# Performance work log

Measured on AMD Instinct MI355X. Metric: run time of the kernel, lower is better.

## Reference

```python
import jax, jax.numpy as jnp
import numpy as np

B, IN_DIM, H, E, V, MAX_LEN = 512, 1024, 512, 512, 2048, 32


def setup_inputs() -> dict:
    key = jax.random.key(0)
    ks = jax.random.split(key, 12)
    s = lambda k, shape, scale: (jax.random.normal(k, shape, dtype=jnp.float32) * scale)
    return {
        'x': jax.random.normal(ks[0], (B, IN_DIM), dtype=jnp.float32),
        'agent_w': s(ks[1], (IN_DIM, H), 1.0 / np.sqrt(IN_DIM)),
        'agent_b': jnp.zeros((H,), jnp.float32),
        'sos_embedding': s(ks[2], (E,), 0.01),  # reset_parameters: normal(0, 0.01)
        'embedding': s(ks[3], (V, E), 1.0),
        'w_ih': s(ks[4], (E, 4 * H), 1.0 / np.sqrt(H)),
        'w_hh': s(ks[5], (H, 4 * H), 1.0 / np.sqrt(H)),
        'b_ih': jnp.zeros((4 * H,), jnp.float32),
        'b_hh': jnp.zeros((4 * H,), jnp.float32),
        'out_w': s(ks[6], (H, V), 1.0 / np.sqrt(H)),
        'out_b': jnp.zeros((V,), jnp.float32),
    }


def _unroll(x, agent_w, agent_b, sos_embedding, embedding, w_ih, w_hh, b_ih, b_hh, out_w, out_b):
    h0 = x @ agent_w + agent_b              # agent provides initial hidden [B, H]
    c0 = jnp.zeros_like(h0)
    e0 = jnp.broadcast_to(sos_embedding, (x.shape[0], sos_embedding.shape[0]))
    key0 = jax.random.key(1)

    def step(carry, _):
        h, c, e, key = carry
        key, sk = jax.random.split(key)
        gates = e @ w_ih + h @ w_hh + (b_ih + b_hh)          # [B, 4H], torch gate order i,f,g,o
        i_g, f_g, g_g, o_g = jnp.split(gates, 4, axis=-1)
        c = jax.nn.sigmoid(f_g) * c + jax.nn.sigmoid(i_g) * jnp.tanh(g_g)
        h = jax.nn.sigmoid(o_g) * jnp.tanh(c)
        step_logits = jax.nn.log_softmax(h @ out_w + out_b, axis=-1)  # [B, V]
        probs = jnp.exp(step_logits)
        entropy = -jnp.sum(probs * step_logits, axis=-1)              # Categorical entropy
        sym = jax.random.categorical(sk, step_logits, axis=-1)        # sample [B]
        log_prob = jnp.take_along_axis(step_logits, sym[:, None], axis=1)[:, 0]
        e = embedding[sym]
        return (h, c, e, key), (sym, log_prob, entropy, probs)

    _, (seq, logp, ent, probs) = jax.lax.scan(step, (h0, c0, e0, key0), None, length=MAX_LEN)
    # scan emits leading time dim -> [B, L, ...]
    seq = jnp.transpose(seq, (1, 0))
    logp = jnp.transpose(logp, (1, 0))
    ent = jnp.transpose(ent, (1, 0))
    probs = jnp.transpose(probs, (1, 0, 2))
    # append EOS step (zeros; probs row of ones, as in the source)
    zcol = jnp.zeros((seq.shape[0], 1), jnp.float32)
    seq = jnp.concatenate([seq, zcol.astype(seq.dtype)], axis=1)
    logp = jnp.concatenate([logp, zcol], axis=1)
    ent = jnp.concatenate([ent, zcol], axis=1)
    probs = jnp.concatenate([probs, jnp.ones((probs.shape[0], 1, probs.shape[2]), probs.dtype)], axis=1)
    return seq, probs, logp, ent


def reference(x, agent_w, agent_b, sos_embedding, embedding, w_ih, w_hh, b_ih, b_hh, out_w, out_b):
    return _unroll(x, agent_w, agent_b, sos_embedding, embedding, w_ih, w_hh, b_ih, b_hh, out_w, out_b)
```

## Files before the change

kernel.cpp:

```cpp
#include <hip/hip_runtime.h>
#include <math.h>
#include <stdint.h>
#include <stddef.h>

#define B_ 512
#define H_ 512
#define E_ 512
#define V_ 2048
#define IN_ 1024
#define LSTEPS 32
#define LP1 33

#define TF_PARTITIONABLE 1

typedef unsigned short u16;
typedef __attribute__((ext_vector_type(8))) short bhalf8;
typedef __attribute__((ext_vector_type(4))) float f32x4;

__device__ __forceinline__ void tf2x32(uint32_t k0, uint32_t k1,
                                       uint32_t x0, uint32_t x1,
                                       uint32_t& o0, uint32_t& o1) {
  uint32_t ks2 = k0 ^ k1 ^ 0x1BD11BDAu;
  x0 += k0; x1 += k1;
#define TFR(R) { x0 += x1; x1 = (x1 << (R)) | (x1 >> (32 - (R))); x1 ^= x0; }
  TFR(13) TFR(15) TFR(26) TFR(6)
  x0 += k1; x1 += ks2 + 1u;
  TFR(17) TFR(29) TFR(16) TFR(24)
  x0 += ks2; x1 += k0 + 2u;
  TFR(13) TFR(15) TFR(26) TFR(6)
  x0 += k0; x1 += k1 + 3u;
  TFR(17) TFR(29) TFR(16) TFR(24)
  x0 += k1; x1 += ks2 + 4u;
  TFR(13) TFR(15) TFR(26) TFR(6)
  x0 += ks2; x1 += k0 + 5u;
#undef TFR
  o0 = x0; o1 = x1;
}

__global__ void init_keys_kernel(uint32_t* __restrict__ sk) {
  uint32_t k0 = 0u, k1 = 1u;
  for (int t = 0; t < LSTEPS; t++) {
    uint32_t a0, a1, b0, b1;
#if TF_PARTITIONABLE
    tf2x32(k0, k1, 0u, 0u, a0, a1);
    tf2x32(k0, k1, 0u, 1u, b0, b1);
    sk[2 * t] = b0; sk[2 * t + 1] = b1;
    k0 = a0; k1 = a1;
#else
    tf2x32(k0, k1, 0u, 2u, a0, a1);
    tf2x32(k0, k1, 1u, 3u, b0, b1);
    sk[2 * t] = a1; sk[2 * t + 1] = b1;
    k0 = a0; k1 = b0;
#endif
  }
}

__device__ __forceinline__ void split3(float v, u16& h, u16& m, u16& l) {
  uint32_t u = __float_as_uint(v);
  uint32_t r = (u + 0x7FFFu + ((u >> 16) & 1u)) >> 16;
  h = (u16)r;
  float res = v - __uint_as_float(r << 16);
  uint32_t u2 = __float_as_uint(res);
  uint32_t r2 = (u2 + 0x7FFFu + ((u2 >> 16) & 1u)) >> 16;
  m = (u16)r2;
  float res2 = res - __uint_as_float(r2 << 16);
  uint32_t u3 = __float_as_uint(res2);
  uint32_t r3 = (u3 + 0x7FFFu + ((u3 >> 16) & 1u)) >> 16;
  l = (u16)r3;
}

__global__ __launch_bounds__(256) void init_state_planes_kernel(
    const float* __restrict__ sos, float* __restrict__ c,
    u16* __restrict__ eh, u16* __restrict__ em, u16* __restrict__ el) {
  int idx = blockIdx.x * 256 + threadIdx.x;
  if (idx < B_ * H_) {
    c[idx] = 0.0f;
    u16 a, b2, d;
    split3(sos[idx & (E_ - 1)], a, b2, d);
    eh[idx] = a; em[idx] = b2; el[idx] = d;
  }
}

__global__ __launch_bounds__(256) void eos_fill_kernel(
    float* __restrict__ o_seq, float* __restrict__ o_probs,
    float* __restrict__ o_logp, float* __restrict__ o_ent) {
  int b = blockIdx.x, tid = threadIdx.x;
  float* pr = o_probs + ((size_t)b * LP1 + LSTEPS) * V_;
  for (int v = tid; v < V_; v += 256) pr[v] = 1.0f;
  if (tid == 0) {
    o_seq[b * LP1 + LSTEPS] = 0.0f;
    o_logp[b * LP1 + LSTEPS] = 0.0f;
    o_ent[b * LP1 + LSTEPS] = 0.0f;
  }
}

__global__ __launch_bounds__(256) void split_kernel(
    const float* __restrict__ src,
    u16* __restrict__ dh, u16* __restrict__ dm, u16* __restrict__ dl, int n) {
  int i = blockIdx.x * 256 + threadIdx.x;
  if (i < n) {
    u16 a, b2, d;
    split3(src[i], a, b2, d);
    dh[i] = a; dm[i] = b2; dl[i] = d;
  }
}

__global__ __launch_bounds__(256) void transpose_split_kernel(
    const float* __restrict__ src, int srcN,
    u16* __restrict__ dh, u16* __restrict__ dm, u16* __restrict__ dl,
    int dstK, int kOff) {
  __shared__ float t[32][33];
  int tx = threadIdx.x & 31, ty = threadIdx.x >> 5;
  int kt = blockIdx.x * 32, nt = blockIdx.y * 32;
#pragma unroll
  for (int j = 0; j < 4; j++)
    t[ty + j * 8][tx] = src[(size_t)(kt + ty + j * 8) * srcN + nt + tx];
  __syncthreads();
#pragma unroll
  for (int j = 0; j < 4; j++) {
    int n = nt + ty + j * 8;
    int k = kt + tx;
    u16 a, b2, d;
    split3(t[tx][ty + j * 8], a, b2, d);
    size_t o = (size_t)n * dstK + kOff + k;
    dh[o] = a; dm[o] = b2; dl[o] = d;
  }
}

typedef __attribute__((address_space(1))) const void GASV;
typedef __attribute__((address_space(3))) void LASV;
__device__ __forceinline__ void gld16(const void* g, void* l) {
  __builtin_amdgcn_global_load_lds((GASV*)g, (LASV*)l, 16, 0, 0);
}

__global__ __launch_bounds__(256, 3) void gemm64_kernel(
    const u16* __restrict__ A0h, const u16* __restrict__ A0m, const u16* __restrict__ A0l,
    const u16* __restrict__ A1h, const u16* __restrict__ A1m, const u16* __restrict__ A1l,
    int strideA, int kHalf,
    const u16* __restrict__ Bh, const u16* __restrict__ Bm, const u16* __restrict__ Bl,
    int strideB, int N, int K, int gridN,
    float* __restrict__ C) {
  __shared__ __align__(16) char lds[2][24576];
  int tid = threadIdx.x;
  int w = tid >> 6, l = tid & 63;
  int bid = blockIdx.x;
  int xcd = bid & 7, mIdx = (bid >> 3) & 7, cIdx = bid >> 6;
  int nIdx = xcd * (gridN >> 3) + cIdx;
  int m0 = mIdx * 64, n0 = nIdx * 64;

  int srow = l >> 2;
  int slog = (l & 3) ^ ((l >> 3) & 3);
  size_t aRow = (size_t)(m0 + w * 16 + srow) * strideA + slog * 8;
  size_t bRow = (size_t)(n0 + w * 16 + srow) * strideB + slog * 8;

  int lrow = l & 15, lk8 = l >> 4;
  int xorv = (lrow >> 1) & 3;
  int wr = (w >> 1) * 32, wc = (w & 1) * 32;
  int fOffA = (wr + lrow) * 64 + ((lk8 ^ xorv) << 4);
  int fOffB = (wc + lrow) * 64 + ((lk8 ^ xorv) << 4);

  f32x4 acc[2][2] = {};
  int nch = K >> 5;

#define STAGE64(CH, TB) {                                               \
    int kc = (CH) << 5;                                                 \
    bool hi2 = kc >= kHalf;                                             \
    const u16* Ah2 = hi2 ? A1h : A0h;                                   \
    const u16* Am2 = hi2 ? A1m : A0m;                                   \
    const u16* Al2 = hi2 ? A1l : A0l;                                   \
    size_t ao = aRow + (hi2 ? kc - kHalf : kc);                         \
    size_t bo = bRow + kc;                                              \
    char* Lb = (char*)&lds[TB][0] + w * 1024;                           \
    gld16(Ah2 + ao, Lb + 0 * 4096);                                     \
    gld16(Am2 + ao, Lb + 1 * 4096);                                     \
    gld16(Al2 + ao, Lb + 2 * 4096);                                     \
    gld16(Bh + bo, Lb + 3 * 4096);                                      \
    gld16(Bm + bo, Lb + 4 * 4096);                                      \
    gld16(Bl + bo, Lb + 5 * 4096);                                      \
  }

  STAGE64(0, 0)
  for (int ch = 0; ch < nch; ch++) {
    __syncthreads();
    if (ch + 1 < nch) STAGE64(ch + 1, (ch + 1) & 1)
    const char* base = (const char*)&lds[ch & 1][0];
    bhalf8 af[3][2], bfr[3][2];
#pragma unroll
    for (int p = 0; p < 3; p++) {
#pragma unroll
      for (int m = 0; m < 2; m++)
        af[p][m] = *(const bhalf8*)(base + p * 4096 + fOffA + m * 1024);
#pragma unroll
      for (int n = 0; n < 2; n++)
        bfr[p][n] = *(const bhalf8*)(base + (3 + p) * 4096 + fOffB + n * 1024);
    }
    const int PA[6] = {2, 0, 1, 1, 0, 0};
    const int PB[6] = {0, 2, 1, 0, 1, 0};
#pragma unroll
    for (int pp = 0; pp < 6; pp++) {
#pragma unroll
      for (int m = 0; m < 2; m++) {
#pragma unroll
        for (int n = 0; n < 2; n++) {
          acc[m][n] = __builtin_amdgcn_mfma_f32_16x16x32_bf16(
              af[PA[pp]][m], bfr[PB[pp]][n], acc[m][n], 0, 0, 0);
        }
      }
    }
  }
#undef STAGE64

#pragma unroll
  for (int m = 0; m < 2; m++) {
#pragma unroll
    for (int n = 0; n < 2; n++) {
#pragma unroll
      for (int j = 0; j < 4; j++) {
        int row = m0 + wr + m * 16 + lk8 * 4 + j;
        int col = n0 + wc + n * 16 + lrow;
        C[(size_t)row * N + col] = acc[m][n][j];
      }
    }
  }
}

__device__ __forceinline__ float sigm(float x) { return 1.0f / (1.0f + expf(-x)); }

__global__ __launch_bounds__(256) void cell_reduce_planes_kernel(
    const float* __restrict__ G,
    const float* __restrict__ b_ih, const float* __restrict__ b_hh,
    float* __restrict__ c,
    u16* __restrict__ hh_, u16* __restrict__ hm_, u16* __restrict__ hl_) {
  int idx = blockIdx.x * 256 + threadIdx.x;
  int b = idx >> 7;
  int h4 = (idx & 127) * 4;
  float4 g4[4];
#pragma unroll
  for (int g = 0; g < 4; g++) {
    size_t off = (size_t)b * 2048 + g * 512 + h4;
    float4 s = *(const float4*)&G[off];
    float4 bi = *(const float4*)&b_ih[g * 512 + h4];
    float4 bh = *(const float4*)&b_hh[g * 512 + h4];
    s.x += bi.x + bh.x; s.y += bi.y + bh.y; s.z += bi.z + bh.z; s.w += bi.w + bh.w;
    g4[g] = s;
  }
  size_t ci = (size_t)b * 512 + h4;
  float4 cold = *(const float4*)&c[ci];
  float4 cn;
  float hv[4];
  {
    const float* ig = (const float*)&g4[0];
    const float* fg = (const float*)&g4[1];
    const float* gg = (const float*)&g4[2];
    const float* og = (const float*)&g4[3];
    float* cc = (float*)&cn;
    const float* co = (const float*)&cold;
#pragma unroll
    for (int k = 0; k < 4; k++) {
      float cv = sigm(fg[k]) * co[k] + sigm(ig[k]) * tanhf(gg[k]);
      cc[k] = cv;
      hv[k] = sigm(og[k]) * tanhf(cv);
    }
  }
  *(float4*)&c[ci] = cn;
  ushort4 vh, vm, vl;
  u16 a, b2, d;
  split3(hv[0], a, b2, d); vh.x = a; vm.x = b2; vl.x = d;
  split3(hv[1], a, b2, d); vh.y = a; vm.y = b2; vl.y = d;
  split3(hv[2], a, b2, d); vh.z = a; vm.z = b2; vl.z = d;
  split3(hv[3], a, b2, d); vh.w = a; vm.w = b2; vl.w = d;
  *(ushort4*)&hh_[ci] = vh;
  *(ushort4*)&hm_[ci] = vm;
  *(ushort4*)&hl_[ci] = vl;
}

__global__ __launch_bounds__(256) void reduce_bias_planes_kernel(
    const float* __restrict__ P, int pstride, int nsplit,
    const float* __restrict__ bias,
    u16* __restrict__ oh, u16* __restrict__ om, u16* __restrict__ ol) {
  int idx = blockIdx.x * 256 + threadIdx.x;
  if (idx >= B_ * H_ / 4) return;
  size_t off = (size_t)idx * 4;
  float4 s = *(const float4*)&P[off];
  for (int sgl = 1; sgl < nsplit; sgl++) {
    float4 p = *(const float4*)&P[(size_t)sgl * pstride + off];
    s.x += p.x; s.y += p.y; s.z += p.z; s.w += p.w;
  }
  int col = (int)(off & (H_ - 1));
  float4 bv = *(const float4*)&bias[col];
  s.x += bv.x; s.y += bv.y; s.z += bv.z; s.w += bv.w;
  ushort4 vh, vm, vl;
  u16 a, b2, d;
  split3(s.x, a, b2, d); vh.x = a; vm.x = b2; vl.x = d;
  split3(s.y, a, b2, d); vh.y = a; vm.y = b2; vl.y = d;
  split3(s.z, a, b2, d); vh.z = a; vm.z = b2; vl.z = d;
  split3(s.w, a, b2, d); vh.w = a; vm.w = b2; vl.w = d;
  *(ushort4*)&oh[off] = vh;
  *(ushort4*)&om[off] = vm;
  *(ushort4*)&ol[off] = vl;
}

__global__ __launch_bounds__(256) void sample_step_kernel(
    const float* __restrict__ Z, const float* __restrict__ out_b,
    const uint32_t* __restrict__ skv,
    const u16* __restrict__ ebH, const u16* __restrict__ ebM, const u16* __restrict__ ebL,
    u16* __restrict__ eh, u16* __restrict__ em_, u16* __restrict__ el_,
    float* __restrict__ o_seq, float* __restrict__ o_probs,
    float* __restrict__ o_logp, float* __restrict__ o_ent, int t) {
  __shared__ float zs[V_];
  __shared__ float rmax[4], rsum[4], rps[4], rav[4];
  __shared__ int rai[4];
  int tid = threadIdx.x, b = blockIdx.x;
  int wid = tid >> 6;
  const float* pr0 = Z + (size_t)b * V_ + tid * 8;
  float4 za = *(const float4*)pr0;
  float4 zb = *(const float4*)(pr0 + 4);
  {
    float4 oa = *(const float4*)(out_b + tid * 8);
    float4 ob = *(const float4*)(out_b + tid * 8 + 4);
    za.x += oa.x; za.y += oa.y; za.z += oa.z; za.w += oa.w;
    zb.x += ob.x; zb.y += ob.y; zb.z += ob.z; zb.w += ob.w;
  }
  float zv[8] = {za.x, za.y, za.z, za.w, zb.x, zb.y, zb.z, zb.w};
  *(float4*)&zs[tid * 8] = za;
  *(float4*)&zs[tid * 8 + 4] = zb;

  float m = zv[0];
#pragma unroll
  for (int i = 1; i < 8; i++) m = fmaxf(m, zv[i]);
  for (int off = 32; off; off >>= 1) m = fmaxf(m, __shfl_xor(m, off));
  if ((tid & 63) == 0) rmax[wid] = m;
  __syncthreads();
  m = fmaxf(fmaxf(rmax[0], rmax[1]), fmaxf(rmax[2], rmax[3]));

  float sh[8];
  float ssum = 0.f;
#pragma unroll
  for (int i = 0; i < 8; i++) { sh[i] = zv[i] - m; ssum += expf(sh[i]); }
  for (int off = 32; off; off >>= 1) ssum += __shfl_xor(ssum, off);
  if ((tid & 63) == 0) rsum[wid] = ssum;
  __syncthreads();
  float S = (rsum[0] + rsum[1]) + (rsum[2] + rsum[3]);
  float ls = logf(S);

  uint32_t sk0 = skv[2 * t], sk1 = skv[2 * t + 1];
  float psum = 0.f;
  float best = -INFINITY;
  int bi = 0;
  float pv[8];
#pragma unroll
  for (int i = 0; i < 8; i++) {
    float s = sh[i] - ls;
    float p = expf(s);
    pv[i] = p;
    psum += p * s;
    int v = tid * 8 + i;
    uint32_t o0, o1, bits;
#if TF_PARTITIONABLE
    uint32_t j = (uint32_t)(b * V_ + v);
    tf2x32(sk0, sk1, 0u, j, o0, o1);
    bits = o0 ^ o1;
#else
    uint32_t j = (uint32_t)(b * V_ + v);
    const uint32_t n2 = (uint32_t)(B_ * V_ / 2);
    if (j < n2) { tf2x32(sk0, sk1, j, j + n2, o0, o1); bits = o0; }
    else       { tf2x32(sk0, sk1, j - n2, j, o0, o1); bits = o1; }
#endif
    float f = __uint_as_float((bits >> 9) | 0x3f800000u) - 1.0f;
    float u = fmaxf(f, 1.17549435e-38f);
    float g = -logf(-logf(u));
    float a = s + g;
    if (a > best) { best = a; bi = v; }
  }
  float* prw = o_probs + ((size_t)b * LP1 + t) * V_ + tid * 8;
  *(float4*)prw = make_float4(pv[0], pv[1], pv[2], pv[3]);
  *(float4*)(prw + 4) = make_float4(pv[4], pv[5], pv[6], pv[7]);

  for (int off = 32; off; off >>= 1) psum += __shfl_xor(psum, off);
  for (int off = 32; off; off >>= 1) {
    float ov = __shfl_xor(best, off);
    int oi = __shfl_xor(bi, off);
    if (ov > best || (ov == best && oi < bi)) { best = ov; bi = oi; }
  }
  if ((tid & 63) == 0) { rps[wid] = psum; rav[wid] = best; rai[wid] = bi; }
  __syncthreads();
  float ent = -((rps[0] + rps[1]) + (rps[2] + rps[3]));
  float bv2 = rav[0]; int sym = rai[0];
#pragma unroll
  for (int w2 = 1; w2 < 4; w2++) {
    if (rav[w2] > bv2 || (rav[w2] == bv2 && rai[w2] < sym)) { bv2 = rav[w2]; sym = rai[w2]; }
  }
  const u16* gh = ebH + (size_t)sym * E_;
  const u16* gm = ebM + (size_t)sym * E_;
  const u16* gl = ebL + (size_t)sym * E_;
  for (int k2 = tid; k2 < E_; k2 += 256) {
    eh[(size_t)b * E_ + k2]  = gh[k2];
    em_[(size_t)b * E_ + k2] = gm[k2];
    el_[(size_t)b * E_ + k2] = gl[k2];
  }
  if (tid == 0) {
    float s_sym = (zs[sym] - m) - ls;
    o_seq[b * LP1 + t] = (float)sym;
    o_logp[b * LP1 + t] = s_sym;
    o_ent[b * LP1 + t] = ent;
  }
}

extern "C" void kernel_launch(void* const* d_in, const int* in_sizes, int n_in,
                              void* d_out, int out_size, void* d_ws, size_t ws_size,
                              hipStream_t stream) {
  (void)in_sizes; (void)n_in; (void)out_size; (void)ws_size;
  const float* x     = (const float*)d_in[0];
  const float* agw   = (const float*)d_in[1];
  const float* agb   = (const float*)d_in[2];
  const float* sos   = (const float*)d_in[3];
  const float* emb   = (const float*)d_in[4];
  const float* w_ih  = (const float*)d_in[5];
  const float* w_hh  = (const float*)d_in[6];
  const float* b_ih  = (const float*)d_in[7];
  const float* b_hh  = (const float*)d_in[8];
  const float* out_w = (const float*)d_in[9];
  const float* out_b = (const float*)d_in[10];

  char* w = (char*)d_ws;
  size_t o = 0;
  uint32_t* sk = (uint32_t*)(w + o); o += 1024;
  float* c = (float*)(w + o);        o += (size_t)B_ * H_ * 4;
#define PLANE3(name, elems) \
  u16* name##H = (u16*)(w + o); o += (size_t)(elems) * 2; \
  u16* name##M = (u16*)(w + o); o += (size_t)(elems) * 2; \
  u16* name##L = (u16*)(w + o); o += (size_t)(elems) * 2;
  PLANE3(e,  B_ * E_)
  PLANE3(hA, B_ * H_)
  PLANE3(hB, B_ * H_)
  PLANE3(xp, B_ * IN_)
  PLANE3(aw, H_ * IN_)
  PLANE3(gw, 2048 * IN_)
  PLANE3(ow, V_ * H_)
  PLANE3(eb, V_ * E_)
#undef PLANE3
  float* P = (float*)(w + o);

  float* out = (float*)d_out;
  float* o_seq   = out;
  float* o_probs = out + (size_t)B_ * LP1;
  float* o_logp  = o_probs + (size_t)B_ * LP1 * V_;
  float* o_ent   = o_logp + (size_t)B_ * LP1;

  const int BIG = 1 << 30;

  init_keys_kernel<<<1, 1, 0, stream>>>(sk);
  init_state_planes_kernel<<<(B_ * H_ + 255) / 256, 256, 0, stream>>>(sos, c, eH, eM, eL);
  eos_fill_kernel<<<B_, 256, 0, stream>>>(o_seq, o_probs, o_logp, o_ent);

  split_kernel<<<(B_ * IN_ + 255) / 256, 256, 0, stream>>>(x, xpH, xpM, xpL, B_ * IN_);
  split_kernel<<<(V_ * E_ + 255) / 256, 256, 0, stream>>>(emb, ebH, ebM, ebL, V_ * E_);
  transpose_split_kernel<<<dim3(512 / 32, 2048 / 32), 256, 0, stream>>>(
      w_ih, 2048, gwH, gwM, gwL, 1024, 0);
  transpose_split_kernel<<<dim3(512 / 32, 2048 / 32), 256, 0, stream>>>(
      w_hh, 2048, gwH, gwM, gwL, 1024, 512);
  transpose_split_kernel<<<dim3(512 / 32, 2048 / 32), 256, 0, stream>>>(
      out_w, 2048, owH, owM, owL, 512, 0);
  transpose_split_kernel<<<dim3(1024 / 32, 512 / 32), 256, 0, stream>>>(
      agw, 512, awH, awM, awL, 1024, 0);

  gemm64_kernel<<<64, 256, 0, stream>>>(
      xpH, xpM, xpL, xpH, xpM, xpL, IN_, BIG,
      awH, awM, awL, IN_, H_, IN_, 8, P);
  reduce_bias_planes_kernel<<<(B_ * H_ / 4 + 255) / 256, 256, 0, stream>>>(
      P, 0, 1, agb, hAH, hAM, hAL);

  for (int t = 0; t < LSTEPS; t++) {
    u16 *hiH = (t & 1) ? hBH : hAH, *hiM = (t & 1) ? hBM : hAM, *hiL = (t & 1) ? hBL : hAL;
    u16 *hoH = (t & 1) ? hAH : hBH, *hoM = (t & 1) ? hAM : hBM, *hoL = (t & 1) ? hAL : hBL;
    gemm64_kernel<<<256, 256, 0, stream>>>(
        eH, eM, eL, hiH, hiM, hiL, E_, E_,
        gwH, gwM, gwL, IN_, 2048, IN_, 32, P);
    cell_reduce_planes_kernel<<<B_ * H_ / 4 / 256, 256, 0, stream>>>(
        P, b_ih, b_hh, c, hoH, hoM, hoL);
    gemm64_kernel<<<256, 256, 0, stream>>>(
        hoH, hoM, hoL, hoH, hoM, hoL, H_, BIG,
        owH, owM, owL, H_, 2048, H_, 32, P);
    sample_step_kernel<<<B_, 256, 0, stream>>>(
        P, out_b, sk, ebH, ebM, ebL, eH, eM, eL,
        o_seq, o_probs, o_logp, o_ent, t);
  }
}
```

Measured before the change: 1.737 ms.

## Fuse recurrent LSTM step loop into one persistent kernel with grid barriers

Replaces the 128 per-step kernel launches (two GEMMs, cell update, sampling per step) with a single persistent kernel of 256 blocks. The phases are separated by a software grid barrier built on an atomic counter. Each block handles two sampling rows. The aim is to remove launch overhead and inter-kernel gaps. In exchange it relies on all 256 blocks being co-resident, and a spin-limit fallback silently skips waiting, which risks wrong results if blocks are not co-resident. Occupancy is also constrained by shared LDS reuse and launch bounds of 2.

```diff
diff --git a/kernel.cpp b/kernel.cpp
--- a/kernel.cpp
+++ b/kernel.cpp
@@ -12,6 +12,9 @@
 #define LP1 33
 
 #define TF_PARTITIONABLE 1
+
+#define NBLOCKS 256
+#define SPIN_LIMIT 500000
 
 typedef unsigned short u16;
 typedef __attribute__((ext_vector_type(8))) short bhalf8;
@@ -37,7 +40,8 @@
   o0 = x0; o1 = x1;
 }
 
-__global__ void init_keys_kernel(uint32_t* __restrict__ sk) {
+__global__ void init_keys_kernel(uint32_t* __restrict__ sk, uint32_t* __restrict__ bar) {
+  bar[0] = 0u;
   uint32_t k0 = 0u, k1 = 1u;
   for (int t = 0; t < LSTEPS; t++) {
     uint32_t a0, a1, b0, b1;
@@ -133,17 +137,34 @@
   __builtin_amdgcn_global_load_lds((GASV*)g, (LASV*)l, 16, 0, 0);
 }
 
-__global__ __launch_bounds__(256, 3) void gemm64_kernel(
-    const u16* __restrict__ A0h, const u16* __restrict__ A0m, const u16* __restrict__ A0l,
-    const u16* __restrict__ A1h, const u16* __restrict__ A1m, const u16* __restrict__ A1l,
+__device__ __forceinline__ void grid_barrier(uint32_t* bar, uint32_t* gen, int* dead) {
+  __syncthreads();
+  if (threadIdx.x == 0) {
+    uint32_t target = (*gen + 1u) * (uint32_t)NBLOCKS;
+    *gen += 1u;
+    __hip_atomic_fetch_add(&bar[0], 1u, __ATOMIC_ACQ_REL, __HIP_MEMORY_SCOPE_SYSTEM);
+    if (!*dead) {
+      int spins = 0;
+      while (__hip_atomic_load(&bar[0], __ATOMIC_ACQUIRE, __HIP_MEMORY_SCOPE_SYSTEM) < target) {
+        __builtin_amdgcn_s_sleep(2);
+        if (++spins > SPIN_LIMIT) { *dead = 1; break; }
+      }
+    }
+  }
+  __syncthreads();
+}
+
+__device__ __forceinline__ void gemm_phase(
+    const u16* A0h, const u16* A0m, const u16* A0l,
+    const u16* A1h, const u16* A1m, const u16* A1l,
     int strideA, int kHalf,
-    const u16* __restrict__ Bh, const u16* __restrict__ Bm, const u16* __restrict__ Bl,
-    int strideB, int N, int K, int gridN,
-    float* __restrict__ C) {
-  __shared__ __align__(16) char lds[2][24576];
+    const u16* Bh, const u16* Bm, const u16* Bl,
+    int strideB, int N, int K,
+    float* C, char* ldsbase) {
   int tid = threadIdx.x;
   int w = tid >> 6, l = tid & 63;
   int bid = blockIdx.x;
+  int gridN = N >> 6;
   int xcd = bid & 7, mIdx = (bid >> 3) & 7, cIdx = bid >> 6;
   int nIdx = xcd * (gridN >> 3) + cIdx;
   int m0 = mIdx * 64, n0 = nIdx * 64;
@@ -162,7 +183,7 @@
   f32x4 acc[2][2] = {};
   int nch = K >> 5;
 
-#define STAGE64(CH, TB) {                                               \
+#define STAGEP(CH, TB) {                                                \
     int kc = (CH) << 5;                                                 \
     bool hi2 = kc >= kHalf;                                             \
     const u16* Ah2 = hi2 ? A1h : A0h;                                   \
@@ -170,7 +191,7 @@
     const u16* Al2 = hi2 ? A1l : A0l;                                   \
     size_t ao = aRow + (hi2 ? kc - kHalf : kc);                         \
     size_t bo = bRow + kc;                                              \
-    char* Lb = (char*)&lds[TB][0] + w * 1024;                           \
+    char* Lb = ldsbase + (TB) * 24576 + w * 1024;                       \
     gld16(Ah2 + ao, Lb + 0 * 4096);                                     \
     gld16(Am2 + ao, Lb + 1 * 4096);                                     \
     gld16(Al2 + ao, Lb + 2 * 4096);                                     \
@@ -179,11 +200,11 @@
     gld16(Bl + bo, Lb + 5 * 4096);                                      \
   }
 
-  STAGE64(0, 0)
+  STAGEP(0, 0)
   for (int ch = 0; ch < nch; ch++) {
     __syncthreads();
-    if (ch + 1 < nch) STAGE64(ch + 1, (ch + 1) & 1)
-    const char* base = (const char*)&lds[ch & 1][0];
+    if (ch + 1 < nch) STAGEP(ch + 1, (ch + 1) & 1)
+    const char* base = ldsbase + (ch & 1) * 24576;
     bhalf8 af[3][2], bfr[3][2];
 #pragma unroll
     for (int p = 0; p < 3; p++) {
@@ -208,8 +229,9 @@
       }
     }
   }
-#undef STAGE64
-
+#undef STAGEP
+
+  __syncthreads();
 #pragma unroll
   for (int m = 0; m < 2; m++) {
 #pragma unroll
@@ -226,11 +248,9 @@
 
 __device__ __forceinline__ float sigm(float x) { return 1.0f / (1.0f + expf(-x)); }
 
-__global__ __launch_bounds__(256) void cell_reduce_planes_kernel(
-    const float* __restrict__ G,
-    const float* __restrict__ b_ih, const float* __restrict__ b_hh,
-    float* __restrict__ c,
-    u16* __restrict__ hh_, u16* __restrict__ hm_, u16* __restrict__ hl_) {
+__device__ __forceinline__ void cell_phase(
+    const float* G, const float* b_ih, const float* b_hh,
+    float* c, u16* hh_, u16* hm_, u16* hl_) {
   int idx = blockIdx.x * 256 + threadIdx.x;
   int b = idx >> 7;
   int h4 = (idx & 127) * 4;
@@ -274,44 +294,15 @@
   *(ushort4*)&hl_[ci] = vl;
 }
 
-__global__ __launch_bounds__(256) void reduce_bias_planes_kernel(
-    const float* __restrict__ P, int pstride, int nsplit,
-    const float* __restrict__ bias,
-    u16* __restrict__ oh, u16* __restrict__ om, u16* __restrict__ ol) {
-  int idx = blockIdx.x * 256 + threadIdx.x;
-  if (idx >= B_ * H_ / 4) return;
-  size_t off = (size_t)idx * 4;
-  float4 s = *(const float4*)&P[off];
-  for (int sgl = 1; sgl < nsplit; sgl++) {
-    float4 p = *(const float4*)&P[(size_t)sgl * pstride + off];
-    s.x += p.x; s.y += p.y; s.z += p.z; s.w += p.w;
-  }
-  int col = (int)(off & (H_ - 1));
-  float4 bv = *(const float4*)&bias[col];
-  s.x += bv.x; s.y += bv.y; s.z += bv.z; s.w += bv.w;
-  ushort4 vh, vm, vl;
-  u16 a, b2, d;
-  split3(s.x, a, b2, d); vh.x = a; vm.x = b2; vl.x = d;
-  split3(s.y, a, b2, d); vh.y = a; vm.y = b2; vl.y = d;
-  split3(s.z, a, b2, d); vh.z = a; vm.z = b2; vl.z = d;
-  split3(s.w, a, b2, d); vh.w = a; vm.w = b2; vl.w = d;
-  *(ushort4*)&oh[off] = vh;
-  *(ushort4*)&om[off] = vm;
-  *(ushort4*)&ol[off] = vl;
-}
-
-__global__ __launch_bounds__(256) void sample_step_kernel(
-    const float* __restrict__ Z, const float* __restrict__ out_b,
-    const uint32_t* __restrict__ skv,
-    const u16* __restrict__ ebH, const u16* __restrict__ ebM, const u16* __restrict__ ebL,
-    u16* __restrict__ eh, u16* __restrict__ em_, u16* __restrict__ el_,
-    float* __restrict__ o_seq, float* __restrict__ o_probs,
-    float* __restrict__ o_logp, float* __restrict__ o_ent, int t) {
-  __shared__ float zs[V_];
-  __shared__ float rmax[4], rsum[4], rps[4], rav[4];
-  __shared__ int rai[4];
-  int tid = threadIdx.x, b = blockIdx.x;
+__device__ __forceinline__ void sample_row(
+    const float* Z, const float* out_b, const uint32_t* skv,
+    const u16* ebH, const u16* ebM, const u16* ebL,
+    u16* eh, u16* em_, u16* el_,
+    float* o_seq, float* o_probs, float* o_logp, float* o_ent, int t, int b,
+    float* zs, float* rmax, float* rsum, float* rps, float* rav, int* rai) {
+  int tid = threadIdx.x;
   int wid = tid >> 6;
+  __syncthreads();
   const float* pr0 = Z + (size_t)b * V_ + tid * 8;
   float4 za = *(const float4*)pr0;
   float4 zb = *(const float4*)(pr0 + 4);
@@ -406,6 +397,179 @@
   }
 }
 
+struct PK {
+  u16 *eH, *eM, *eL;
+  u16 *hAH, *hAM, *hAL;
+  u16 *hBH, *hBM, *hBL;
+  const u16 *gwH, *gwM, *gwL;
+  const u16 *owH, *owM, *owL;
+  const u16 *ebH, *ebM, *ebL;
+  const float *b_ih, *b_hh, *out_b;
+  float *c, *G;
+  const uint32_t* sk;
+  uint32_t* bar;
+  float *o_seq, *o_probs, *o_logp, *o_ent;
+};
+
+__global__ __launch_bounds__(256, 2) void rnn_persistent_kernel(PK p) {
+  __shared__ __align__(16) char smem[2 * 24576];
+  __shared__ float rmax[4], rsum[4], rps[4], rav[4];
+  __shared__ int rai[4];
+  __shared__ uint32_t bgen;
+  __shared__ int bdead;
+  char* glds = smem;
+  float* zs = (float*)smem;
+
+  if (threadIdx.x == 0) { bgen = 0u; bdead = 0; }
+  __syncthreads();
+
+  u16 *hiH = p.hAH, *hiM = p.hAM, *hiL = p.hAL;
+  u16 *hoH = p.hBH, *hoM = p.hBM, *hoL = p.hBL;
+
+  for (int t = 0; t < LSTEPS; t++) {
+    gemm_phase(p.eH, p.eM, p.eL, hiH, hiM, hiL, E_, E_,
+               p.gwH, p.gwM, p.gwL, IN_, 2048, IN_, p.G, glds);
+    grid_barrier(p.bar, &bgen, &bdead);
+
+    cell_phase(p.G, p.b_ih, p.b_hh, p.c, hoH, hoM, hoL);
+    grid_barrier(p.bar, &bgen, &bdead);
+
+    gemm_phase(hoH, hoM, hoL, hoH, hoM, hoL, H_, 1 << 30,
+               p.owH, p.owM, p.owL, H_, 2048, H_, p.G, glds);
+    grid_barrier(p.bar, &bgen, &bdead);
+
+    sample_row(p.G, p.out_b, p.sk, p.ebH, p.ebM, p.ebL,
+               p.eH, p.eM, p.eL, p.o_seq, p.o_probs, p.o_logp, p.o_ent,
+               t, blockIdx.x * 2 + 0, zs, rmax, rsum, rps, rav, rai);
+    sample_row(p.G, p.out_b, p.sk, p.ebH, p.ebM, p.ebL,
+               p.eH, p.eM, p.eL, p.o_seq, p.o_probs, p.o_logp, p.o_ent,
+               t, blockIdx.x * 2 + 1, zs, rmax, rsum, rps, rav, rai);
+    grid_barrier(p.bar, &bgen, &bdead);
+
+    u16* tp;
+    tp = hiH; hiH = hoH; hoH = tp;
+    tp = hiM; hiM = hoM; hoM = tp;
+    tp = hiL; hiL = hoL; hoL = tp;
+  }
+}
+
+__global__ __launch_bounds__(256, 3) void gemm64_kernel(
+    const u16* __restrict__ A0h, const u16* __restrict__ A0m, const u16* __restrict__ A0l,
+    const u16* __restrict__ A1h, const u16* __restrict__ A1m, const u16* __restrict__ A1l,
+    int strideA, int kHalf,
+    const u16* __restrict__ Bh, const u16* __restrict__ Bm, const u16* __restrict__ Bl,
+    int strideB, int N, int K, int gridN,
+    float* __restrict__ C) {
+  __shared__ __align__(16) char lds[2][24576];
+  int tid = threadIdx.x;
+  int w = tid >> 6, l = tid & 63;
+  int bid = blockIdx.x;
+  int xcd = bid & 7, mIdx = (bid >> 3) & 7, cIdx = bid >> 6;
+  int nIdx = xcd * (gridN >> 3) + cIdx;
+  int m0 = mIdx * 64, n0 = nIdx * 64;
+
+  int srow = l >> 2;
+  int slog = (l & 3) ^ ((l >> 3) & 3);
+  size_t aRow = (size_t)(m0 + w * 16 + srow) * strideA + slog * 8;
+  size_t bRow = (size_t)(n0 + w * 16 + srow) * strideB + slog * 8;
+
+  int lrow = l & 15, lk8 = l >> 4;
+  int xorv = (lrow >> 1) & 3;
+  int wr = (w >> 1) * 32, wc = (w & 1) * 32;
+  int fOffA = (wr + lrow) * 64 + ((lk8 ^ xorv) << 4);
+  int fOffB = (wc + lrow) * 64 + ((lk8 ^ xorv) << 4);
+
+  f32x4 acc[2][2] = {};
+  int nch = K >> 5;
+
+#define STAGE64(CH, TB) {                                               \
+    int kc = (CH) << 5;                                                 \
+    bool hi2 = kc >= kHalf;                                             \
+    const u16* Ah2 = hi2 ? A1h : A0h;                                   \
+    const u16* Am2 = hi2 ? A1m : A0m;                                   \
+    const u16* Al2 = hi2 ? A1l : A0l;                                   \
+    size_t ao = aRow + (hi2 ? kc - kHalf : kc);                         \
+    size_t bo = bRow + kc;                                              \
+    char* Lb = (char*)&lds[TB][0] + w * 1024;                           \
+    gld16(Ah2 + ao, Lb + 0 * 4096);                                     \
+    gld16(Am2 + ao, Lb + 1 * 4096);                                     \
+    gld16(Al2 + ao, Lb + 2 * 4096);                                     \
+    gld16(Bh + bo, Lb + 3 * 4096);                                      \
+    gld16(Bm + bo, Lb + 4 * 4096);                                      \
+    gld16(Bl + bo, Lb + 5 * 4096);                                      \
+  }
+
+  STAGE64(0, 0)
+  for (int ch = 0; ch < nch; ch++) {
+    __syncthreads();
+    if (ch + 1 < nch) STAGE64(ch + 1, (ch + 1) & 1)
+    const char* base = (const char*)&lds[ch & 1][0];
+    bhalf8 af[3][2], bfr[3][2];
+#pragma unroll
+    for (int p = 0; p < 3; p++) {
+#pragma unroll
+      for (int m = 0; m < 2; m++)
+        af[p][m] = *(const bhalf8*)(base + p * 4096 + fOffA + m * 1024);
+#pragma unroll
+      for (int n = 0; n < 2; n++)
+        bfr[p][n] = *(const bhalf8*)(base + (3 + p) * 4096 + fOffB + n * 1024);
+    }
+    const int PA[6] = {2, 0, 1, 1, 0, 0};
+    const int PB[6] = {0, 2, 1, 0, 1, 0};
+#pragma unroll
+    for (int pp = 0; pp < 6; pp++) {
+#pragma unroll
+      for (int m = 0; m < 2; m++) {
+#pragma unroll
+        for (int n = 0; n < 2; n++) {
+          acc[m][n] = __builtin_amdgcn_mfma_f32_16x16x32_bf16(
+              af[PA[pp]][m], bfr[PB[pp]][n], acc[m][n], 0, 0, 0);
+        }
+      }
+    }
+  }
+#undef STAGE64
+
+#pragma unroll
+  for (int m = 0; m < 2; m++) {
+#pragma unroll
+    for (int n = 0; n < 2; n++) {
+#pragma unroll
+      for (int j = 0; j < 4; j++) {
+        int row = m0 + wr + m * 16 + lk8 * 4 + j;
+        int col = n0 + wc + n * 16 + lrow;
+        C[(size_t)row * N + col] = acc[m][n][j];
+      }
+    }
+  }
+}
+
+__global__ __launch_bounds__(256) void reduce_bias_planes_kernel(
+    const float* __restrict__ P, int pstride, int nsplit,
+    const float* __restrict__ bias,
+    u16* __restrict__ oh, u16* __restrict__ om, u16* __restrict__ ol) {
+  int idx = blockIdx.x * 256 + threadIdx.x;
+  if (idx >= B_ * H_ / 4) return;
+  size_t off = (size_t)idx * 4;
+  float4 s = *(const float4*)&P[off];
+  for (int sgl = 1; sgl < nsplit; sgl++) {
+    float4 p = *(const float4*)&P[(size_t)sgl * pstride + off];
+    s.x += p.x; s.y += p.y; s.z += p.z; s.w += p.w;
+  }
+  int col = (int)(off & (H_ - 1));
+  float4 bv = *(const float4*)&bias[col];
+  s.x += bv.x; s.y += bv.y; s.z += bv.z; s.w += bv.w;
+  ushort4 vh, vm, vl;
+  u16 a, b2, d;
+  split3(s.x, a, b2, d); vh.x = a; vm.x = b2; vl.x = d;
+  split3(s.y, a, b2, d); vh.y = a; vm.y = b2; vl.y = d;
+  split3(s.z, a, b2, d); vh.z = a; vm.z = b2; vl.z = d;
+  split3(s.w, a, b2, d); vh.w = a; vm.w = b2; vl.w = d;
+  *(ushort4*)&oh[off] = vh;
+  *(ushort4*)&om[off] = vm;
+  *(ushort4*)&ol[off] = vl;
+}
+
 extern "C" void kernel_launch(void* const* d_in, const int* in_sizes, int n_in,
                               void* d_out, int out_size, void* d_ws, size_t ws_size,
                               hipStream_t stream) {
@@ -424,7 +588,9 @@
 
   char* w = (char*)d_ws;
   size_t o = 0;
-  uint32_t* sk = (uint32_t*)(w + o); o += 1024;
+  uint32_t* sk = (uint32_t*)(w + o);
+  uint32_t* bar = (uint32_t*)(w + 512);
+  o += 1024;
   float* c = (float*)(w + o);        o += (size_t)B_ * H_ * 4;
 #define PLANE3(name, elems) \
   u16* name##H = (u16*)(w + o); o += (size_t)(elems) * 2; \
@@ -449,7 +615,7 @@
 
   const int BIG = 1 << 30;
 
-  init_keys_kernel<<<1, 1, 0, stream>>>(sk);
+  init_keys_kernel<<<1, 1, 0, stream>>>(sk, bar);
   init_state_planes_kernel<<<(B_ * H_ + 255) / 256, 256, 0, stream>>>(sos, c, eH, eM, eL);
   eos_fill_kernel<<<B_, 256, 0, stream>>>(o_seq, o_probs, o_logp, o_ent);
 
@@ -470,19 +636,15 @@
   reduce_bias_planes_kernel<<<(B_ * H_ / 4 + 255) / 256, 256, 0, stream>>>(
       P, 0, 1, agb, hAH, hAM, hAL);
 
-  for (int t = 0; t < LSTEPS; t++) {
-    u16 *hiH = (t & 1) ? hBH : hAH, *hiM = (t & 1) ? hBM : hAM, *hiL = (t & 1) ? hBL : hAL;
-    u16 *hoH = (t & 1) ? hAH : hBH, *hoM = (t & 1) ? hAM : hBM, *hoL = (t & 1) ? hAL : hBL;
-    gemm64_kernel<<<256, 256, 0, stream>>>(
-        eH, eM, eL, hiH, hiM, hiL, E_, E_,
-        gwH, gwM, gwL, IN_, 2048, IN_, 32, P);
-    cell_reduce_planes_kernel<<<B_ * H_ / 4 / 256, 256, 0, stream>>>(
-        P, b_ih, b_hh, c, hoH, hoM, hoL);
-    gemm64_kernel<<<256, 256, 0, stream>>>(
-        hoH, hoM, hoL, hoH, hoM, hoL, H_, BIG,
-        owH, owM, owL, H_, 2048, H_, 32, P);
-    sample_step_kernel<<<B_, 256, 0, stream>>>(
-        P, out_b, sk, ebH, ebM, ebL, eH, eM, eL,
-        o_seq, o_probs, o_logp, o_ent, t);
-  }
-}
+  PK pk;
+  pk.eH = eH; pk.eM = eM; pk.eL = eL;
+  pk.hAH = hAH; pk.hAM = hAM; pk.hAL = hAL;
+  pk.hBH = hBH; pk.hBM = hBM; pk.hBL = hBL;
+  pk.gwH = gwH; pk.gwM = gwM; pk.gwL = gwL;
+  pk.owH = owH; pk.owM = owM; pk.owL = owL;
+  pk.ebH = ebH; pk.ebM = ebM; pk.ebL = ebL;
+  pk.b_ih = b_ih; pk.b_hh = b_hh; pk.out_b = out_b;
+  pk.c = c; pk.G = P; pk.sk = sk; pk.bar = bar;
+  pk.o_seq = o_seq; pk.o_probs = o_probs; pk.o_logp = o_logp; pk.o_ent = o_ent;
+  rnn_persistent_kernel<<<NBLOCKS, 256, 0, stream>>>(pk);
+}
```

Result: slower. 4.014 ms (+131.1%).

## Fuse LSTM cell update into gates GEMM epilogue via interleaved gate weight layout

Applied to the files above, without the earlier changes.

Weight rows for the gate GEMM are reordered so that the four gates of each hidden unit sit in adjacent columns. Each 64-column output tile then holds complete i,f,g,o sets for 16 hidden units, so the LSTM cell update can run in the GEMM epilogue through an LDS staging tile. This drops the separate cell kernel launch per step and the round trip of the 4MB gate matrix through global memory. Bias sums are prepacked once into the interleaved order. The epilogue does scalar stores of c and h with less coalescing than before.

```diff
diff --git a/kernel.cpp b/kernel.cpp
--- a/kernel.cpp
+++ b/kernel.cpp
@@ -105,10 +105,18 @@
   }
 }
 
+__global__ __launch_bounds__(256) void bias_pack_kernel(
+    const float* __restrict__ b_ih, const float* __restrict__ b_hh,
+    float* __restrict__ bsum) {
+  int n = blockIdx.x * 256 + threadIdx.x;
+  int h = n >> 2, g = n & 3;
+  bsum[n] = b_ih[g * 512 + h] + b_hh[g * 512 + h];
+}
+
 __global__ __launch_bounds__(256) void transpose_split_kernel(
     const float* __restrict__ src, int srcN,
     u16* __restrict__ dh, u16* __restrict__ dm, u16* __restrict__ dl,
-    int dstK, int kOff) {
+    int dstK, int kOff, int gateRemap) {
   __shared__ float t[32][33];
   int tx = threadIdx.x & 31, ty = threadIdx.x >> 5;
   int kt = blockIdx.x * 32, nt = blockIdx.y * 32;
@@ -120,9 +128,10 @@
   for (int j = 0; j < 4; j++) {
     int n = nt + ty + j * 8;
     int k = kt + tx;
+    int nrow = gateRemap ? (((n & 511) << 2) | (n >> 9)) : n;
     u16 a, b2, d;
     split3(t[tx][ty + j * 8], a, b2, d);
-    size_t o = (size_t)n * dstK + kOff + k;
+    size_t o = (size_t)nrow * dstK + kOff + k;
     dh[o] = a; dm[o] = b2; dl[o] = d;
   }
 }
@@ -132,84 +141,87 @@
 __device__ __forceinline__ void gld16(const void* g, void* l) {
   __builtin_amdgcn_global_load_lds((GASV*)g, (LASV*)l, 16, 0, 0);
 }
+
+__device__ __forceinline__ float sigm(float x) { return 1.0f / (1.0f + expf(-x)); }
+
+#define GEMM_DECODE(N_)                                                     \
+  int tid = threadIdx.x;                                                    \
+  int w = tid >> 6, l = tid & 63;                                           \
+  int bid = blockIdx.x;                                                     \
+  int gridN = (N_) >> 6;                                                    \
+  int xcd = bid & 7, mIdx = (bid >> 3) & 7, cIdx = bid >> 6;                \
+  int nIdx = xcd * (gridN >> 3) + cIdx;                                     \
+  int m0 = mIdx * 64, n0 = nIdx * 64;                                       \
+  int srow = l >> 2;                                                        \
+  int slog = (l & 3) ^ ((l >> 3) & 3);                                      \
+  int lrow = l & 15, lk8 = l >> 4;                                          \
+  int xorv = (lrow >> 1) & 3;                                               \
+  int wr = (w >> 1) * 32, wc = (w & 1) * 32;                                \
+  int fOffA = (wr + lrow) * 64 + ((lk8 ^ xorv) << 4);                       \
+  int fOffB = (wc + lrow) * 64 + ((lk8 ^ xorv) << 4);
+
+#define STAGE6(CH, TB, LDSB)  {                                             \
+    int kc = (CH) << 5;                                                     \
+    bool hi2 = kc >= kHalf;                                                 \
+    const u16* Ah2 = hi2 ? A1h : A0h;                                       \
+    const u16* Am2 = hi2 ? A1m : A0m;                                       \
+    const u16* Al2 = hi2 ? A1l : A0l;                                       \
+    size_t ao = aRow + (hi2 ? kc - kHalf : kc);                             \
+    size_t bo = bRow + kc;                                                  \
+    char* Lb = (LDSB) + (TB) * 24576 + w * 1024;                            \
+    gld16(Ah2 + ao, Lb + 0 * 4096);                                         \
+    gld16(Am2 + ao, Lb + 1 * 4096);                                         \
+    gld16(Al2 + ao, Lb + 2 * 4096);                                         \
+    gld16(Bh + bo, Lb + 3 * 4096);                                          \
+    gld16(Bm + bo, Lb + 4 * 4096);                                          \
+    gld16(Bl + bo, Lb + 5 * 4096);                                          \
+  }
+
+#define GEMM_KLOOP(LDSB)                                                    \
+  STAGE6(0, 0, LDSB)                                                        \
+  for (int ch = 0; ch < nch; ch++) {                                        \
+    __syncthreads();                                                        \
+    if (ch + 1 < nch) STAGE6(ch + 1, (ch + 1) & 1, LDSB)                    \
+    const char* base = (LDSB) + (ch & 1) * 24576;                           \
+    bhalf8 af[3][2], bfr[3][2];                                             \
+    _Pragma("unroll")                                                       \
+    for (int p = 0; p < 3; p++) {                                           \
+      _Pragma("unroll")                                                     \
+      for (int m = 0; m < 2; m++)                                           \
+        af[p][m] = *(const bhalf8*)(base + p * 4096 + fOffA + m * 1024);    \
+      _Pragma("unroll")                                                     \
+      for (int n = 0; n < 2; n++)                                           \
+        bfr[p][n] = *(const bhalf8*)(base + (3 + p) * 4096 + fOffB + n * 1024); \
+    }                                                                       \
+    const int PA[6] = {2, 0, 1, 1, 0, 0};                                   \
+    const int PB[6] = {0, 2, 1, 0, 1, 0};                                   \
+    _Pragma("unroll")                                                       \
+    for (int pp = 0; pp < 6; pp++) {                                        \
+      _Pragma("unroll")                                                     \
+      for (int m = 0; m < 2; m++) {                                         \
+        _Pragma("unroll")                                                   \
+        for (int n = 0; n < 2; n++) {                                       \
+          acc[m][n] = __builtin_amdgcn_mfma_f32_16x16x32_bf16(              \
+              af[PA[pp]][m], bfr[PB[pp]][n], acc[m][n], 0, 0, 0);           \
+        }                                                                   \
+      }                                                                     \
+    }                                                                       \
+  }
 
 __global__ __launch_bounds__(256, 3) void gemm64_kernel(
     const u16* __restrict__ A0h, const u16* __restrict__ A0m, const u16* __restrict__ A0l,
     const u16* __restrict__ A1h, const u16* __restrict__ A1m, const u16* __restrict__ A1l,
     int strideA, int kHalf,
     const u16* __restrict__ Bh, const u16* __restrict__ Bm, const u16* __restrict__ Bl,
-    int strideB, int N, int K, int gridN,
+    int strideB, int N, int K,
     float* __restrict__ C) {
   __shared__ __align__(16) char lds[2][24576];
-  int tid = threadIdx.x;
-  int w = tid >> 6, l = tid & 63;
-  int bid = blockIdx.x;
-  int xcd = bid & 7, mIdx = (bid >> 3) & 7, cIdx = bid >> 6;
-  int nIdx = xcd * (gridN >> 3) + cIdx;
-  int m0 = mIdx * 64, n0 = nIdx * 64;
-
-  int srow = l >> 2;
-  int slog = (l & 3) ^ ((l >> 3) & 3);
+  GEMM_DECODE(N)
   size_t aRow = (size_t)(m0 + w * 16 + srow) * strideA + slog * 8;
   size_t bRow = (size_t)(n0 + w * 16 + srow) * strideB + slog * 8;
-
-  int lrow = l & 15, lk8 = l >> 4;
-  int xorv = (lrow >> 1) & 3;
-  int wr = (w >> 1) * 32, wc = (w & 1) * 32;
-  int fOffA = (wr + lrow) * 64 + ((lk8 ^ xorv) << 4);
-  int fOffB = (wc + lrow) * 64 + ((lk8 ^ xorv) << 4);
-
   f32x4 acc[2][2] = {};
   int nch = K >> 5;
-
-#define STAGE64(CH, TB) {                                               \
-    int kc = (CH) << 5;                                                 \
-    bool hi2 = kc >= kHalf;                                             \
-    const u16* Ah2 = hi2 ? A1h : A0h;                                   \
-    const u16* Am2 = hi2 ? A1m : A0m;                                   \
-    const u16* Al2 = hi2 ? A1l : A0l;                                   \
-    size_t ao = aRow + (hi2 ? kc - kHalf : kc);                         \
-    size_t bo = bRow + kc;                                              \
-    char* Lb = (char*)&lds[TB][0] + w * 1024;                           \
-    gld16(Ah2 + ao, Lb + 0 * 4096);                                     \
-    gld16(Am2 + ao, Lb + 1 * 4096);                                     \
-    gld16(Al2 + ao, Lb + 2 * 4096);                                     \
-    gld16(Bh + bo, Lb + 3 * 4096);                                      \
-    gld16(Bm + bo, Lb + 4 * 4096);                                      \
-    gld16(Bl + bo, Lb + 5 * 4096);                                      \
-  }
-
-  STAGE64(0, 0)
-  for (int ch = 0; ch < nch; ch++) {
-    __syncthreads();
-    if (ch + 1 < nch) STAGE64(ch + 1, (ch + 1) & 1)
-    const char* base = (const char*)&lds[ch & 1][0];
-    bhalf8 af[3][2], bfr[3][2];
-#pragma unroll
-    for (int p = 0; p < 3; p++) {
-#pragma unroll
-      for (int m = 0; m < 2; m++)
-        af[p][m] = *(const bhalf8*)(base + p * 4096 + fOffA + m * 1024);
-#pragma unroll
-      for (int n = 0; n < 2; n++)
-        bfr[p][n] = *(const bhalf8*)(base + (3 + p) * 4096 + fOffB + n * 1024);
-    }
-    const int PA[6] = {2, 0, 1, 1, 0, 0};
-    const int PB[6] = {0, 2, 1, 0, 1, 0};
-#pragma unroll
-    for (int pp = 0; pp < 6; pp++) {
-#pragma unroll
-      for (int m = 0; m < 2; m++) {
-#pragma unroll
-        for (int n = 0; n < 2; n++) {
-          acc[m][n] = __builtin_amdgcn_mfma_f32_16x16x32_bf16(
-              af[PA[pp]][m], bfr[PB[pp]][n], acc[m][n], 0, 0, 0);
-        }
-      }
-    }
-  }
-#undef STAGE64
-
+  GEMM_KLOOP((char*)&lds[0][0])
 #pragma unroll
   for (int m = 0; m < 2; m++) {
 #pragma unroll
@@ -224,54 +236,54 @@
   }
 }
 
-__device__ __forceinline__ float sigm(float x) { return 1.0f / (1.0f + expf(-x)); }
-
-__global__ __launch_bounds__(256) void cell_reduce_planes_kernel(
-    const float* __restrict__ G,
-    const float* __restrict__ b_ih, const float* __restrict__ b_hh,
+__global__ __launch_bounds__(256, 3) void gemm_gates_cell_kernel(
+    const u16* __restrict__ A0h, const u16* __restrict__ A0m, const u16* __restrict__ A0l,
+    const u16* __restrict__ A1h, const u16* __restrict__ A1m, const u16* __restrict__ A1l,
+    const u16* __restrict__ Bh, const u16* __restrict__ Bm, const u16* __restrict__ Bl,
+    const float* __restrict__ bsum,
     float* __restrict__ c,
-    u16* __restrict__ hh_, u16* __restrict__ hm_, u16* __restrict__ hl_) {
-  int idx = blockIdx.x * 256 + threadIdx.x;
-  int b = idx >> 7;
-  int h4 = (idx & 127) * 4;
-  float4 g4[4];
-#pragma unroll
-  for (int g = 0; g < 4; g++) {
-    size_t off = (size_t)b * 2048 + g * 512 + h4;
-    float4 s = *(const float4*)&G[off];
-    float4 bi = *(const float4*)&b_ih[g * 512 + h4];
-    float4 bh = *(const float4*)&b_hh[g * 512 + h4];
-    s.x += bi.x + bh.x; s.y += bi.y + bh.y; s.z += bi.z + bh.z; s.w += bi.w + bh.w;
-    g4[g] = s;
-  }
-  size_t ci = (size_t)b * 512 + h4;
-  float4 cold = *(const float4*)&c[ci];
-  float4 cn;
-  float hv[4];
-  {
-    const float* ig = (const float*)&g4[0];
-    const float* fg = (const float*)&g4[1];
-    const float* gg = (const float*)&g4[2];
-    const float* og = (const float*)&g4[3];
-    float* cc = (float*)&cn;
-    const float* co = (const float*)&cold;
-#pragma unroll
-    for (int k = 0; k < 4; k++) {
-      float cv = sigm(fg[k]) * co[k] + sigm(ig[k]) * tanhf(gg[k]);
-      cc[k] = cv;
-      hv[k] = sigm(og[k]) * tanhf(cv);
+    u16* __restrict__ hoH, u16* __restrict__ hoM, u16* __restrict__ hoL) {
+  __shared__ __align__(16) char lds[2][24576];
+  const int strideA = E_, strideB = IN_, kHalf = E_;
+  GEMM_DECODE(2048)
+  size_t aRow = (size_t)(m0 + w * 16 + srow) * strideA + slog * 8;
+  size_t bRow = (size_t)(n0 + w * 16 + srow) * strideB + slog * 8;
+  f32x4 acc[2][2] = {};
+  int nch = IN_ >> 5;
+  GEMM_KLOOP((char*)&lds[0][0])
+
+  __syncthreads();
+  float* tile = (float*)&lds[0][0];
+#pragma unroll
+  for (int m = 0; m < 2; m++) {
+#pragma unroll
+    for (int n = 0; n < 2; n++) {
+#pragma unroll
+      for (int j = 0; j < 4; j++) {
+        int r = wr + m * 16 + lk8 * 4 + j;
+        int cc = wc + n * 16 + lrow;
+        tile[r * 68 + cc] = acc[m][n][j];
+      }
     }
   }
-  *(float4*)&c[ci] = cn;
-  ushort4 vh, vm, vl;
-  u16 a, b2, d;
-  split3(hv[0], a, b2, d); vh.x = a; vm.x = b2; vl.x = d;
-  split3(hv[1], a, b2, d); vh.y = a; vm.y = b2; vl.y = d;
-  split3(hv[2], a, b2, d); vh.z = a; vm.z = b2; vl.z = d;
-  split3(hv[3], a, b2, d); vh.w = a; vm.w = b2; vl.w = d;
-  *(ushort4*)&hh_[ci] = vh;
-  *(ushort4*)&hm_[ci] = vm;
-  *(ushort4*)&hl_[ci] = vl;
+  __syncthreads();
+  int hbase = n0 >> 2;
+#pragma unroll
+  for (int p = 0; p < 4; p++) {
+    int id = tid + p * 256;
+    int bl = id >> 4, hl = id & 15;
+    float4 g = *(float4*)&tile[bl * 68 + hl * 4];
+    float4 bs = *(const float4*)&bsum[n0 + hl * 4];
+    float ig = g.x + bs.x, fg = g.y + bs.y, gg = g.z + bs.z, og = g.w + bs.w;
+    size_t ci = (size_t)(m0 + bl) * 512 + hbase + hl;
+    float cold = c[ci];
+    float cv = sigm(fg) * cold + sigm(ig) * tanhf(gg);
+    float hv = sigm(og) * tanhf(cv);
+    c[ci] = cv;
+    u16 a, b2, d;
+    split3(hv, a, b2, d);
+    hoH[ci] = a; hoM[ci] = b2; hoL[ci] = d;
+  }
 }
 
 __global__ __launch_bounds__(256) void reduce_bias_planes_kernel(
@@ -423,8 +435,9 @@
   const float* out_b = (const float*)d_in[10];
 
   char* w = (char*)d_ws;
-  size_t o = 0;
-  uint32_t* sk = (uint32_t*)(w + o); o += 1024;
+  uint32_t* sk = (uint32_t*)w;
+  float* bsum = (float*)(w + 4096);
+  size_t o = 4096 + 8192;
   float* c = (float*)(w + o);        o += (size_t)B_ * H_ * 4;
 #define PLANE3(name, elems) \
   u16* name##H = (u16*)(w + o); o += (size_t)(elems) * 2; \
@@ -452,35 +465,34 @@
   init_keys_kernel<<<1, 1, 0, stream>>>(sk);
   init_state_planes_kernel<<<(B_ * H_ + 255) / 256, 256, 0, stream>>>(sos, c, eH, eM, eL);
   eos_fill_kernel<<<B_, 256, 0, stream>>>(o_seq, o_probs, o_logp, o_ent);
+  bias_pack_kernel<<<8, 256, 0, stream>>>(b_ih, b_hh, bsum);
 
   split_kernel<<<(B_ * IN_ + 255) / 256, 256, 0, stream>>>(x, xpH, xpM, xpL, B_ * IN_);
   split_kernel<<<(V_ * E_ + 255) / 256, 256, 0, stream>>>(emb, ebH, ebM, ebL, V_ * E_);
   transpose_split_kernel<<<dim3(512 / 32, 2048 / 32), 256, 0, stream>>>(
-      w_ih, 2048, gwH, gwM, gwL, 1024, 0);
+      w_ih, 2048, gwH, gwM, gwL, 1024, 0, 1);
   transpose_split_kernel<<<dim3(512 / 32, 2048 / 32), 256, 0, stream>>>(
-      w_hh, 2048, gwH, gwM, gwL, 1024, 512);
+      w_hh, 2048, gwH, gwM, gwL, 1024, 512, 1);
   transpose_split_kernel<<<dim3(512 / 32, 2048 / 32), 256, 0, stream>>>(
-      out_w, 2048, owH, owM, owL, 512, 0);
+      out_w, 2048, owH, owM, owL, 512, 0, 0);
   transpose_split_kernel<<<dim3(1024 / 32, 512 / 32), 256, 0, stream>>>(
-      agw, 512, awH, awM, awL, 1024, 0);
+      agw, 512, awH, awM, awL, 1024, 0, 0);
 
   gemm64_kernel<<<64, 256, 0, stream>>>(
       xpH, xpM, xpL, xpH, xpM, xpL, IN_, BIG,
-      awH, awM, awL, IN_, H_, IN_, 8, P);
+      awH, awM, awL, IN_, H_, IN_, P);
   reduce_bias_planes_kernel<<<(B_ * H_ / 4 + 255) / 256, 256, 0, stream>>>(
       P, 0, 1, agb, hAH, hAM, hAL);
 
   for (int t = 0; t < LSTEPS; t++) {
     u16 *hiH = (t & 1) ? hBH : hAH, *hiM = (t & 1) ? hBM : hAM, *hiL = (t & 1) ? hBL : hAL;
     u16 *hoH = (t & 1) ? hAH : hBH, *hoM = (t & 1) ? hAM : hBM, *hoL = (t & 1) ? hAL : hBL;
-    gemm64_kernel<<<256, 256, 0, stream>>>(
-        eH, eM, eL, hiH, hiM, hiL, E_, E_,
-        gwH, gwM, gwL, IN_, 2048, IN_, 32, P);
-    cell_reduce_planes_kernel<<<B_ * H_ / 4 / 256, 256, 0, stream>>>(
-        P, b_ih, b_hh, c, hoH, hoM, hoL);
+    gemm_gates_cell_kernel<<<256, 256, 0, stream>>>(
+        eH, eM, eL, hiH, hiM, hiL,
+        gwH, gwM, gwL, bsum, c, hoH, hoM, hoL);
     gemm64_kernel<<<256, 256, 0, stream>>>(
         hoH, hoM, hoL, hoH, hoM, hoL, H_, BIG,
-        owH, owM, owL, H_, 2048, H_, 32, P);
+        owH, owM, owL, H_, 2048, H_, P);
     sample_step_kernel<<<B_, 256, 0, stream>>>(
         P, out_b, sk, ebH, ebM, ebL, eH, eM, eL,
         o_seq, o_probs, o_logp, o_ent, t);
```

Measured after the change: 1.601 ms. 7.9% less time.
